# Performance work log

Measured on AMD Instinct MI355X. Metric: run time of the kernel, lower is better.

The kernel has to match this reference:

```python
import jax, jax.numpy as jnp
import numpy as np
import math

D_MODEL, N_HEADS, D_HEAD = 1024, 16, 64
INIT_RANGE = 0.02
IGNORE = -100000.0


def setup_inputs() -> dict:
    key = jax.random.key(0)
    ks = jax.random.split(key, 5)
    x = jax.random.normal(ks[0], (2, 2048, D_MODEL), dtype=jnp.float32)
    W_Q = INIT_RANGE * jax.random.normal(ks[1], (N_HEADS, D_MODEL, D_HEAD), dtype=jnp.float32)
    W_K = INIT_RANGE * jax.random.normal(ks[2], (N_HEADS, D_MODEL, D_HEAD), dtype=jnp.float32)
    W_V = INIT_RANGE * jax.random.normal(ks[3], (N_HEADS, D_MODEL, D_HEAD), dtype=jnp.float32)
    # W_O is contracted as 'n_heads d_head d_model' in the original einsum
    W_O = INIT_RANGE * jax.random.normal(ks[4], (N_HEADS, D_HEAD, D_MODEL), dtype=jnp.float32)
    b_Q = jnp.zeros((N_HEADS, D_HEAD), dtype=jnp.float32)
    b_K = jnp.zeros((N_HEADS, D_HEAD), dtype=jnp.float32)
    b_V = jnp.zeros((N_HEADS, D_HEAD), dtype=jnp.float32)
    b_O = jnp.zeros((D_MODEL,), dtype=jnp.float32)
    return {"normalized_resid_pre": x, "W_Q": W_Q, "b_Q": b_Q, "W_K": W_K, "b_K": b_K,
            "W_V": W_V, "b_V": b_V, "W_O": W_O, "b_O": b_O}


def reference(normalized_resid_pre, W_Q, b_Q, W_K, b_K, W_V, b_V, W_O, b_O):
    x = normalized_resid_pre  # [b, s, d_model]
    q = jnp.einsum('bsd,hde->bshe', x, W_Q) + b_Q  # [b, s, h, d_head]
    k = jnp.einsum('bsd,hde->bshe', x, W_K) + b_K
    v = jnp.einsum('bsd,hde->bshe', x, W_V) + b_V
    scores = jnp.einsum('bqhe,bkhe->bhqk', q, k) / math.sqrt(D_HEAD)
    S = x.shape[1]
    causal = jnp.tril(jnp.ones((S, S), dtype=bool))  # True where allowed
    scores = jnp.where(causal, scores, IGNORE)
    pattern = jax.nn.softmax(scores, axis=-1)  # [b, h, q, k]
    z = jnp.einsum('bhqk,bkhe->bqhe', pattern, v)
    attn_out = jnp.einsum('bqhe,hed->bqd', z, W_O) + b_O
    return attn_out
```

## Files before the change

kernel.cpp:

```cpp
#include <hip/hip_runtime.h>
#include <cstdint>
#include <cstddef>

typedef unsigned short u16;
typedef __bf16 bf16x8 __attribute__((ext_vector_type(8)));
typedef _Float16 f16x4 __attribute__((ext_vector_type(4)));
typedef _Float16 f16x2 __attribute__((ext_vector_type(2)));
typedef float  f32x4  __attribute__((ext_vector_type(4)));
typedef unsigned short u16x8 __attribute__((ext_vector_type(8)));
typedef unsigned short u16x4 __attribute__((ext_vector_type(4)));

#define DM   1024
#define NH   16
#define DH   64
#define SS   2048
#define BSZ  4096
#define NQKV 3072
#define QSCALE 0.18033688011f

__device__ __forceinline__ u16 f2b(float f) {
  unsigned u = __builtin_bit_cast(unsigned, f);
  return (u16)((u + 0x7FFFu + ((u >> 16) & 1u)) >> 16);
}
__device__ __forceinline__ u16 f2h(float f) {
  _Float16 h = (_Float16)f;
  return __builtin_bit_cast(u16, h);
}

__device__ __forceinline__ void gl_lds16(const void* g, void* l) {
  __builtin_amdgcn_global_load_lds(
      (__attribute__((address_space(1))) void*)(void*)g,
      (__attribute__((address_space(3))) void*)l, 16, 0, 0);
}

__global__ __launch_bounds__(256) void prep_all_kernel(
    const float* __restrict__ x, u16* __restrict__ xb,
    const float* __restrict__ Wq, const float* __restrict__ Wk,
    const float* __restrict__ Wv, u16* __restrict__ wqkvt,
    const float* __restrict__ Wo, u16* __restrict__ wot) {
  __shared__ __align__(16) u16 Ts[64 * 72];
  int bid = blockIdx.x, t = threadIdx.x;
  if (bid < 2048) {
    int i = (bid * 256 + t) * 8;
    float4 a = *(const float4*)(x + i);
    float4 b = *(const float4*)(x + i + 4);
    u16x8 o;
    o[0] = f2b(a.x); o[1] = f2b(a.y); o[2] = f2b(a.z); o[3] = f2b(a.w);
    o[4] = f2b(b.x); o[5] = f2b(b.y); o[6] = f2b(b.z); o[7] = f2b(b.w);
    *(u16x8*)(xb + i) = o;
    return;
  }
  if (bid < 2816) {
    int idx = bid - 2048;
    int dt = idx & 15, sl = idx >> 4;
    int proj = sl >> 4, h = sl & 15;
    const float* W = (proj == 0) ? Wq : ((proj == 1) ? Wk : Wv);
    int d0 = dt * 64;
    {
      int ld = t >> 2;
      int ec = (t & 3) * 16;
      const float* src = W + ((size_t)h * DM + d0 + ld) * DH + ec;
      float4 v0 = *(const float4*)(src);
      float4 v1 = *(const float4*)(src + 4);
      float4 v2 = *(const float4*)(src + 8);
      float4 v3 = *(const float4*)(src + 12);
      float vv[16] = {v0.x, v0.y, v0.z, v0.w, v1.x, v1.y, v1.z, v1.w,
                      v2.x, v2.y, v2.z, v2.w, v3.x, v3.y, v3.z, v3.w};
#pragma unroll
      for (int i = 0; i < 16; i++) Ts[(ec + i) * 72 + ld] = f2b(vv[i]);
    }
    __syncthreads();
    {
      int le = t >> 2;
      int dc = (t & 3) * 16;
      int n = proj * DM + h * DH + le;
      u16* dst = wqkvt + (size_t)n * DM + d0 + dc;
      *(u16x8*)(dst)     = *(const u16x8*)&Ts[le * 72 + dc];
      *(u16x8*)(dst + 8) = *(const u16x8*)&Ts[le * 72 + dc + 8];
    }
    return;
  }
  {
    int idx = bid - 2816;
    int dt = idx & 15, h = idx >> 4;
    int d0 = dt * 64;
    {
      int le = t >> 2;
      int dc = (t & 3) * 16;
      const float* src = Wo + ((size_t)h * DH + le) * DM + d0 + dc;
      float4 v0 = *(const float4*)(src);
      float4 v1 = *(const float4*)(src + 4);
      float4 v2 = *(const float4*)(src + 8);
      float4 v3 = *(const float4*)(src + 12);
      float vv[16] = {v0.x, v0.y, v0.z, v0.w, v1.x, v1.y, v1.z, v1.w,
                      v2.x, v2.y, v2.z, v2.w, v3.x, v3.y, v3.z, v3.w};
#pragma unroll
      for (int i = 0; i < 16; i++) Ts[(dc + i) * 72 + le] = f2b(vv[i]);
    }
    __syncthreads();
    {
      int ld = t >> 2;
      int ec = (t & 3) * 16;
      u16* dst = wot + (size_t)(d0 + ld) * DM + h * DH + ec;
      *(u16x8*)(dst)     = *(const u16x8*)&Ts[ld * 72 + ec];
      *(u16x8*)(dst + 8) = *(const u16x8*)&Ts[ld * 72 + ec + 8];
    }
  }
}

__global__ __launch_bounds__(256) void gemm_qkv_kernel(
    const u16* __restrict__ A, const u16* __restrict__ Bt,
    u16* __restrict__ o_q, u16* __restrict__ o_k, u16* __restrict__ o_v,
    const float* __restrict__ c0, const float* __restrict__ c1,
    const float* __restrict__ c2) {
  const int K = DM;
  __shared__ __align__(16) u16 As[128 * 32];
  __shared__ __align__(16) u16 Bs[128 * 32];
  __shared__ __align__(16) u16 Cs[64 * 128];
  int t = threadIdx.x, w = t >> 6, l = t & 63;
  int lr = l & 15, lq = l >> 4;
  int m0 = blockIdx.x * 128, n0 = blockIdx.y * 128;
  int wr = w >> 1, wc = w & 1;
  f32x4 acc[4][4] = {};
  const u16* ga = A + (size_t)(m0 + (t >> 2)) * K + (t & 3) * 8;
  const u16* gb = Bt + (size_t)(n0 + (t >> 2)) * K + (t & 3) * 8;

  for (int k0 = 0; k0 < K; k0 += 32) {
    __syncthreads();
    gl_lds16(ga + k0,           &As[w * 512]);
    gl_lds16(ga + k0 + 64 * K,  &As[2048 + w * 512]);
    gl_lds16(gb + k0,           &Bs[w * 512]);
    gl_lds16(gb + k0 + 64 * K,  &Bs[2048 + w * 512]);
    __syncthreads();
    bf16x8 af[4], bfr[4];
#pragma unroll
    for (int i = 0; i < 4; i++)
      af[i] = *(const bf16x8*)&As[(wr * 64 + i * 16 + lr) * 32 + lq * 8];
#pragma unroll
    for (int j = 0; j < 4; j++)
      bfr[j] = *(const bf16x8*)&Bs[(wc * 64 + j * 16 + lr) * 32 + lq * 8];
#pragma unroll
    for (int i = 0; i < 4; i++)
#pragma unroll
      for (int j = 0; j < 4; j++)
        acc[i][j] = __builtin_amdgcn_mfma_f32_16x16x32_bf16(af[i], bfr[j], acc[i][j], 0, 0, 0);
  }

  int proj = n0 >> 10;
  int r0 = n0 & 1023;
  int h0 = r0 >> 6;
  const float* bp = (proj == 0) ? c0 : ((proj == 1) ? c1 : c2);

#pragma unroll
  for (int p = 0; p < 2; p++) {
    __syncthreads();
    if (wr == p) {
#pragma unroll
      for (int j = 0; j < 4; j++) {
        int nl = wc * 64 + j * 16 + lr;
        float bias = bp[r0 + nl];
#pragma unroll
        for (int i = 0; i < 4; i++) {
#pragma unroll
          for (int g = 0; g < 4; g++) {
            int ml = i * 16 + lq * 4 + g;
            float val = acc[i][j][g] + bias;
            if (proj == 0)      Cs[ml * 128 + nl] = f2b(val * QSCALE);
            else if (proj == 1) Cs[ml * 128 + nl] = f2b(val);
            else                Cs[nl * 64 + ml] = f2h(val);
          }
        }
      }
    }
    __syncthreads();
    int m_base = m0 + p * 64;
    if (proj < 2) {
      int ml = t >> 2, q4 = t & 3;
      int hh = q4 >> 1, e0 = (q4 & 1) * 32;
      int m = m_base + ml, b = m >> 11, s = m & 2047;
      int h = h0 + hh;
      u16* dst = (proj == 0 ? o_q : o_k) + ((size_t)(b * NH + h) * SS + s) * DH + e0;
      const u16* src = &Cs[ml * 128 + hh * 64 + e0];
      *(u16x8*)(dst)      = *(const u16x8*)(src);
      *(u16x8*)(dst + 8)  = *(const u16x8*)(src + 8);
      *(u16x8*)(dst + 16) = *(const u16x8*)(src + 16);
      *(u16x8*)(dst + 24) = *(const u16x8*)(src + 24);
    } else {
      int er = t >> 1, sh = t & 1;
      int hh = er >> 6, e = er & 63;
      int h = h0 + hh;
      int ms = m_base + sh * 32, b = ms >> 11, s = ms & 2047;
      u16* dst = o_v + ((size_t)(b * NH + h) * DH + e) * SS + s;
      const u16* src = &Cs[er * 64 + sh * 32];
      *(u16x8*)(dst)      = *(const u16x8*)(src);
      *(u16x8*)(dst + 8)  = *(const u16x8*)(src + 8);
      *(u16x8*)(dst + 16) = *(const u16x8*)(src + 16);
      *(u16x8*)(dst + 24) = *(const u16x8*)(src + 24);
    }
  }
}

__global__ __launch_bounds__(256) void gemm_o_kernel(
    const u16* __restrict__ A, const u16* __restrict__ Bt,
    const float* __restrict__ bo, float* __restrict__ fout) {
  const int K = DM;
  __shared__ __align__(16) u16 As[128 * 32];
  __shared__ __align__(16) u16 Bs[64 * 32];
  int t = threadIdx.x, w = t >> 6, l = t & 63;
  int lr = l & 15, lq = l >> 4;
  int m0 = blockIdx.x * 128, n0 = blockIdx.y * 64;
  f32x4 acc[2][4] = {};
  const u16* ga = A + (size_t)(m0 + (t >> 2)) * K + (t & 3) * 8;
  const u16* gb = Bt + (size_t)(n0 + (t >> 2)) * K + (t & 3) * 8;

  for (int k0 = 0; k0 < K; k0 += 32) {
    __syncthreads();
    gl_lds16(ga + k0,           &As[w * 512]);
    gl_lds16(ga + k0 + 64 * K,  &As[2048 + w * 512]);
    gl_lds16(gb + k0, &Bs[w * 512]);
    __syncthreads();
    bf16x8 af[2], bfr[4];
#pragma unroll
    for (int i = 0; i < 2; i++)
      af[i] = *(const bf16x8*)&As[(w * 32 + i * 16 + lr) * 32 + lq * 8];
#pragma unroll
    for (int j = 0; j < 4; j++)
      bfr[j] = *(const bf16x8*)&Bs[(j * 16 + lr) * 32 + lq * 8];
#pragma unroll
    for (int i = 0; i < 2; i++)
#pragma unroll
      for (int j = 0; j < 4; j++)
        acc[i][j] = __builtin_amdgcn_mfma_f32_16x16x32_bf16(af[i], bfr[j], acc[i][j], 0, 0, 0);
  }

  int mb = m0 + w * 32 + lq * 4;
  int nb = n0 + lr;
#pragma unroll
  for (int j = 0; j < 4; j++) {
    int n = nb + j * 16;
    float bias = bo[n];
#pragma unroll
    for (int i = 0; i < 2; i++) {
#pragma unroll
      for (int g = 0; g < 4; g++) {
        int m = mb + i * 16 + g;
        fout[(size_t)m * DM + n] = acc[i][j][g] + bias;
      }
    }
  }
}

__global__ __launch_bounds__(512) void attn_kernel(const u16* __restrict__ q_ws,
                                                   const u16* __restrict__ k_ws,
                                                   const u16* __restrict__ vt_ws,
                                                   u16* __restrict__ z_ws) {
  __shared__ __align__(16) u16 KsA[2][64 * 72], VsA[2][64 * 72];
  __shared__ __align__(16) u16 KsB[2][64 * 72], VsB[2][64 * 72];
  __shared__ float lbuf[2][64];

  int t = threadIdx.x;
  int g = t >> 8;
  int tl = t & 255;
  int w4 = tl >> 6;
  int l = t & 63;
  int lr = l & 15, lq = l >> 4;
  int srow = tl >> 3;
  int sc8 = (tl & 7) * 8;

  u16 (*Ks)[64 * 72] = g ? KsB : KsA;
  u16 (*Vs)[64 * 72] = g ? VsB : VsA;

  int bid = blockIdx.x;
  int xcd = bid & 7, idx = bid >> 3;
  int bh = xcd * 4 + (idx & 3);
  int j = idx >> 2;
  const u16* Qb = q_ws + (size_t)bh * SS * DH;
  const u16* Kb = k_ws + (size_t)bh * SS * DH;
  const u16* Vb = vt_ws + (size_t)bh * DH * SS;
  int b = bh >> 4, h16 = bh & 15;

  const f16x4 ones = {(_Float16)1.f, (_Float16)1.f, (_Float16)1.f, (_Float16)1.f};

  for (int half = 0; half < 2; half++) {
    int qt = half ? (31 - j) : j;
    int q0 = qt * 64;
    int nkt = qt + 1;
    int h = nkt >> 1;
    int cnt1 = nkt - h;
    int mycnt = g ? cnt1 : h;
    int base = g ? h : 0;

    int qrow = q0 + w4 * 16 + lr;
    bf16x8 qf0 = *(const bf16x8*)(Qb + (size_t)qrow * DH + lq * 8);
    bf16x8 qf1 = *(const bf16x8*)(Qb + (size_t)qrow * DH + 32 + lq * 8);

    f32x4 accO[4] = {};
    f32x4 accL = {};

    __syncthreads();
    if (mycnt > 0) {
      int k0 = base * 64;
      const u16* kg = Kb + (size_t)(k0 + srow) * DH + sc8;
      const u16* vg = Vb + (size_t)srow * SS + k0 + sc8;
      u16x8 r0 = *(const u16x8*)kg;
      u16x8 r1 = *(const u16x8*)(kg + 32 * DH);
      u16x8 r2 = *(const u16x8*)vg;
      u16x8 r3 = *(const u16x8*)(vg + 32 * SS);
      *(u16x8*)&Ks[0][srow * 72 + sc8] = r0;
      *(u16x8*)&Ks[0][(srow + 32) * 72 + sc8] = r1;
      *(u16x8*)&Vs[0][srow * 72 + sc8] = r2;
      *(u16x8*)&Vs[0][(srow + 32) * 72 + sc8] = r3;
    }

    for (int it = 0; it < cnt1; ++it) {
      __syncthreads();
      bool act = it < mycnt;
      int pb = it & 1;

      u16x8 r0, r1, r2, r3;
      bool have_next = (it + 1 < mycnt);
      if (have_next) {
        int k0n = (base + it + 1) * 64;
        const u16* kg = Kb + (size_t)(k0n + srow) * DH + sc8;
        const u16* vg = Vb + (size_t)srow * SS + k0n + sc8;
        r0 = *(const u16x8*)kg;
        r1 = *(const u16x8*)(kg + 32 * DH);
        r2 = *(const u16x8*)vg;
        r3 = *(const u16x8*)(vg + 32 * SS);
      }

      if (act) {
        f32x4 sc[4];
#pragma unroll
        for (int nt = 0; nt < 4; nt++) {
          bf16x8 kf0 = *(const bf16x8*)&Ks[pb][(nt * 16 + lr) * 72 + lq * 8];
          bf16x8 kf1 = *(const bf16x8*)&Ks[pb][(nt * 16 + lr) * 72 + 32 + lq * 8];
          f32x4 a = {0.f, 0.f, 0.f, 0.f};
          a = __builtin_amdgcn_mfma_f32_16x16x32_bf16(kf0, qf0, a, 0, 0, 0);
          a = __builtin_amdgcn_mfma_f32_16x16x32_bf16(kf1, qf1, a, 0, 0, 0);
          sc[nt] = a;
        }

        if (g == 1 && it == cnt1 - 1) {
          int k0 = (base + it) * 64;
          int gq = q0 + w4 * 16 + lr;
#pragma unroll
          for (int nt = 0; nt < 4; nt++) {
#pragma unroll
            for (int gg = 0; gg < 4; gg++) {
              int gk = k0 + nt * 16 + lq * 4 + gg;
              if (gk > gq) sc[nt][gg] = -1e30f;
            }
          }
        }

        f16x4 pf[4];
#pragma unroll
        for (int nt = 0; nt < 4; nt++) {
          float p0 = exp2f(sc[nt][0]);
          float p1 = exp2f(sc[nt][1]);
          float p2 = exp2f(sc[nt][2]);
          float p3 = exp2f(sc[nt][3]);
          f16x2 e0 = __builtin_bit_cast(f16x2, __builtin_amdgcn_cvt_pkrtz(p0, p1));
          f16x2 e1 = __builtin_bit_cast(f16x2, __builtin_amdgcn_cvt_pkrtz(p2, p3));
          pf[nt][0] = e0[0]; pf[nt][1] = e0[1];
          pf[nt][2] = e1[0]; pf[nt][3] = e1[1];
        }

#pragma unroll
        for (int ks = 0; ks < 4; ks++) {
          accL = __builtin_amdgcn_mfma_f32_16x16x16f16(ones, pf[ks], accL, 0, 0, 0);
#pragma unroll
          for (int et = 0; et < 4; et++) {
            f16x4 vf = *(const f16x4*)&Vs[pb][(et * 16 + lr) * 72 + ks * 16 + lq * 4];
            accO[et] = __builtin_amdgcn_mfma_f32_16x16x16f16(vf, pf[ks], accO[et], 0, 0, 0);
          }
        }
      }

      if (have_next) {
        int nb2 = (it + 1) & 1;
        *(u16x8*)&Ks[nb2][srow * 72 + sc8] = r0;
        *(u16x8*)&Ks[nb2][(srow + 32) * 72 + sc8] = r1;
        *(u16x8*)&Vs[nb2][srow * 72 + sc8] = r2;
        *(u16x8*)&Vs[nb2][(srow + 32) * 72 + sc8] = r3;
      }
    }

    __syncthreads();
    if (lq == 0) lbuf[g][w4 * 16 + lr] = accL[0];
    __syncthreads();
    float inv = 1.0f / (accL[0] + lbuf[1 - g][w4 * 16 + lr]);

    float* cbuf = (float*)VsB[1];
    int gq = q0 + w4 * 16 + lr;
    int crow = w4 * 16 + lr;
    u16* zrow = z_ws + ((size_t)(b * SS + gq)) * DM + h16 * DH;
#pragma unroll
    for (int c = 0; c < 2; c++) {
      if (g == 1) {
#pragma unroll
        for (int e2 = 0; e2 < 2; e2++) {
          int et = 2 * c + e2;
#pragma unroll
          for (int gg = 0; gg < 4; gg++)
            cbuf[crow * 32 + e2 * 16 + lq * 4 + gg] = accO[et][gg];
        }
      }
      __syncthreads();
      if (g == 0) {
#pragma unroll
        for (int e2 = 0; e2 < 2; e2++) {
          int et = 2 * c + e2;
          u16x4 o;
#pragma unroll
          for (int gg = 0; gg < 4; gg++) {
            float v = accO[et][gg] + cbuf[crow * 32 + e2 * 16 + lq * 4 + gg];
            o[gg] = f2b(v * inv);
          }
          *(u16x4*)(zrow + et * 16 + lq * 4) = o;
        }
      }
      __syncthreads();
    }
  }
}

extern "C" void kernel_launch(void* const* d_in, const int* in_sizes, int n_in,
                              void* d_out, int out_size, void* d_ws, size_t ws_size,
                              hipStream_t stream) {
  const float* x  = (const float*)d_in[0];
  const float* Wq = (const float*)d_in[1];
  const float* bq = (const float*)d_in[2];
  const float* Wk = (const float*)d_in[3];
  const float* bk = (const float*)d_in[4];
  const float* Wv = (const float*)d_in[5];
  const float* bv = (const float*)d_in[6];
  const float* Wo = (const float*)d_in[7];
  const float* bo = (const float*)d_in[8];
  float* out = (float*)d_out;

  char* ws = (char*)d_ws;
  const size_t MB = 1u << 20;
  u16* xb    = (u16*)(ws);
  u16* wqkvt = (u16*)(ws + 8 * MB);
  u16* wot   = (u16*)(ws + 14 * MB);
  u16* q_ws  = (u16*)(ws + 16 * MB);
  u16* k_ws  = (u16*)(ws + 24 * MB);
  u16* vt_ws = (u16*)(ws + 32 * MB);
  u16* z_ws  = (u16*)(ws + 40 * MB);

  prep_all_kernel<<<3072, 256, 0, stream>>>(x, xb, Wq, Wk, Wv, wqkvt, Wo, wot);

  gemm_qkv_kernel<<<dim3(BSZ / 128, NQKV / 128), 256, 0, stream>>>(
      xb, wqkvt, q_ws, k_ws, vt_ws, bq, bk, bv);

  attn_kernel<<<512, 512, 0, stream>>>(q_ws, k_ws, vt_ws, z_ws);

  gemm_o_kernel<<<dim3(BSZ / 128, DM / 64), 256, 0, stream>>>(z_ws, wot, bo, out);
}
```

Before: 191.8 us.

## Give each attention block one query tile instead of split-KV paired tiles

```diff
diff --git a/kernel.cpp b/kernel.cpp
--- a/kernel.cpp
+++ b/kernel.cpp
@@ -250,30 +250,23 @@
   }
 }
 
-__global__ __launch_bounds__(512) void attn_kernel(const u16* __restrict__ q_ws,
+__global__ __launch_bounds__(256) void attn_kernel(const u16* __restrict__ q_ws,
                                                    const u16* __restrict__ k_ws,
                                                    const u16* __restrict__ vt_ws,
                                                    u16* __restrict__ z_ws) {
-  __shared__ __align__(16) u16 KsA[2][64 * 72], VsA[2][64 * 72];
-  __shared__ __align__(16) u16 KsB[2][64 * 72], VsB[2][64 * 72];
-  __shared__ float lbuf[2][64];
+  __shared__ __align__(16) u16 Ks[2][64 * 72], Vs[2][64 * 72];
 
   int t = threadIdx.x;
-  int g = t >> 8;
-  int tl = t & 255;
-  int w4 = tl >> 6;
+  int w = t >> 6;
   int l = t & 63;
   int lr = l & 15, lq = l >> 4;
-  int srow = tl >> 3;
-  int sc8 = (tl & 7) * 8;
-
-  u16 (*Ks)[64 * 72] = g ? KsB : KsA;
-  u16 (*Vs)[64 * 72] = g ? VsB : VsA;
+  int srow = t >> 3;
+  int sc8 = (t & 7) * 8;
 
   int bid = blockIdx.x;
   int xcd = bid & 7, idx = bid >> 3;
   int bh = xcd * 4 + (idx & 3);
-  int j = idx >> 2;
+  int qt = 31 - (idx >> 2);
   const u16* Qb = q_ws + (size_t)bh * SS * DH;
   const u16* Kb = k_ws + (size_t)bh * SS * DH;
   const u16* Vb = vt_ws + (size_t)bh * DH * SS;
@@ -281,148 +274,104 @@
 
   const f16x4 ones = {(_Float16)1.f, (_Float16)1.f, (_Float16)1.f, (_Float16)1.f};
 
-  for (int half = 0; half < 2; half++) {
-    int qt = half ? (31 - j) : j;
-    int q0 = qt * 64;
-    int nkt = qt + 1;
-    int h = nkt >> 1;
-    int cnt1 = nkt - h;
-    int mycnt = g ? cnt1 : h;
-    int base = g ? h : 0;
-
-    int qrow = q0 + w4 * 16 + lr;
-    bf16x8 qf0 = *(const bf16x8*)(Qb + (size_t)qrow * DH + lq * 8);
-    bf16x8 qf1 = *(const bf16x8*)(Qb + (size_t)qrow * DH + 32 + lq * 8);
-
-    f32x4 accO[4] = {};
-    f32x4 accL = {};
-
-    __syncthreads();
-    if (mycnt > 0) {
-      int k0 = base * 64;
-      const u16* kg = Kb + (size_t)(k0 + srow) * DH + sc8;
-      const u16* vg = Vb + (size_t)srow * SS + k0 + sc8;
-      u16x8 r0 = *(const u16x8*)kg;
-      u16x8 r1 = *(const u16x8*)(kg + 32 * DH);
-      u16x8 r2 = *(const u16x8*)vg;
-      u16x8 r3 = *(const u16x8*)(vg + 32 * SS);
-      *(u16x8*)&Ks[0][srow * 72 + sc8] = r0;
-      *(u16x8*)&Ks[0][(srow + 32) * 72 + sc8] = r1;
-      *(u16x8*)&Vs[0][srow * 72 + sc8] = r2;
-      *(u16x8*)&Vs[0][(srow + 32) * 72 + sc8] = r3;
-    }
-
-    for (int it = 0; it < cnt1; ++it) {
-      __syncthreads();
-      bool act = it < mycnt;
-      int pb = it & 1;
-
-      u16x8 r0, r1, r2, r3;
-      bool have_next = (it + 1 < mycnt);
-      if (have_next) {
-        int k0n = (base + it + 1) * 64;
-        const u16* kg = Kb + (size_t)(k0n + srow) * DH + sc8;
-        const u16* vg = Vb + (size_t)srow * SS + k0n + sc8;
-        r0 = *(const u16x8*)kg;
-        r1 = *(const u16x8*)(kg + 32 * DH);
-        r2 = *(const u16x8*)vg;
-        r3 = *(const u16x8*)(vg + 32 * SS);
-      }
-
-      if (act) {
-        f32x4 sc[4];
-#pragma unroll
-        for (int nt = 0; nt < 4; nt++) {
-          bf16x8 kf0 = *(const bf16x8*)&Ks[pb][(nt * 16 + lr) * 72 + lq * 8];
-          bf16x8 kf1 = *(const bf16x8*)&Ks[pb][(nt * 16 + lr) * 72 + 32 + lq * 8];
-          f32x4 a = {0.f, 0.f, 0.f, 0.f};
-          a = __builtin_amdgcn_mfma_f32_16x16x32_bf16(kf0, qf0, a, 0, 0, 0);
-          a = __builtin_amdgcn_mfma_f32_16x16x32_bf16(kf1, qf1, a, 0, 0, 0);
-          sc[nt] = a;
-        }
-
-        if (g == 1 && it == cnt1 - 1) {
-          int k0 = (base + it) * 64;
-          int gq = q0 + w4 * 16 + lr;
-#pragma unroll
-          for (int nt = 0; nt < 4; nt++) {
-#pragma unroll
-            for (int gg = 0; gg < 4; gg++) {
-              int gk = k0 + nt * 16 + lq * 4 + gg;
-              if (gk > gq) sc[nt][gg] = -1e30f;
-            }
-          }
-        }
-
-        f16x4 pf[4];
-#pragma unroll
-        for (int nt = 0; nt < 4; nt++) {
-          float p0 = exp2f(sc[nt][0]);
-          float p1 = exp2f(sc[nt][1]);
-          float p2 = exp2f(sc[nt][2]);
-          float p3 = exp2f(sc[nt][3]);
-          f16x2 e0 = __builtin_bit_cast(f16x2, __builtin_amdgcn_cvt_pkrtz(p0, p1));
-          f16x2 e1 = __builtin_bit_cast(f16x2, __builtin_amdgcn_cvt_pkrtz(p2, p3));
-          pf[nt][0] = e0[0]; pf[nt][1] = e0[1];
-          pf[nt][2] = e1[0]; pf[nt][3] = e1[1];
-        }
-
-#pragma unroll
-        for (int ks = 0; ks < 4; ks++) {
-          accL = __builtin_amdgcn_mfma_f32_16x16x16f16(ones, pf[ks], accL, 0, 0, 0);
-#pragma unroll
-          for (int et = 0; et < 4; et++) {
-            f16x4 vf = *(const f16x4*)&Vs[pb][(et * 16 + lr) * 72 + ks * 16 + lq * 4];
-            accO[et] = __builtin_amdgcn_mfma_f32_16x16x16f16(vf, pf[ks], accO[et], 0, 0, 0);
-          }
+  int q0 = qt * 64;
+  int nkt = qt + 1;
+
+  int qrow = q0 + w * 16 + lr;
+  bf16x8 qf0 = *(const bf16x8*)(Qb + (size_t)qrow * DH + lq * 8);
+  bf16x8 qf1 = *(const bf16x8*)(Qb + (size_t)qrow * DH + 32 + lq * 8);
+
+  f32x4 accO[4] = {};
+  f32x4 accL = {};
+
+  {
+    const u16* kg = Kb + (size_t)srow * DH + sc8;
+    const u16* vg = Vb + (size_t)srow * SS + sc8;
+    *(u16x8*)&Ks[0][srow * 72 + sc8] = *(const u16x8*)kg;
+    *(u16x8*)&Ks[0][(srow + 32) * 72 + sc8] = *(const u16x8*)(kg + 32 * DH);
+    *(u16x8*)&Vs[0][srow * 72 + sc8] = *(const u16x8*)vg;
+    *(u16x8*)&Vs[0][(srow + 32) * 72 + sc8] = *(const u16x8*)(vg + 32 * SS);
+  }
+
+  for (int it = 0; it < nkt; ++it) {
+    __syncthreads();
+    int pb = it & 1;
+    bool have_next = (it + 1 < nkt);
+
+    u16x8 r0, r1, r2, r3;
+    if (have_next) {
+      int k0n = (it + 1) * 64;
+      const u16* kg = Kb + (size_t)(k0n + srow) * DH + sc8;
+      const u16* vg = Vb + (size_t)srow * SS + k0n + sc8;
+      r0 = *(const u16x8*)kg;
+      r1 = *(const u16x8*)(kg + 32 * DH);
+      r2 = *(const u16x8*)vg;
+      r3 = *(const u16x8*)(vg + 32 * SS);
+    }
+
+    f32x4 sc[4];
+#pragma unroll
+    for (int nt = 0; nt < 4; nt++) {
+      bf16x8 kf0 = *(const bf16x8*)&Ks[pb][(nt * 16 + lr) * 72 + lq * 8];
+      bf16x8 kf1 = *(const bf16x8*)&Ks[pb][(nt * 16 + lr) * 72 + 32 + lq * 8];
+      f32x4 a = {0.f, 0.f, 0.f, 0.f};
+      a = __builtin_amdgcn_mfma_f32_16x16x32_bf16(kf0, qf0, a, 0, 0, 0);
+      a = __builtin_amdgcn_mfma_f32_16x16x32_bf16(kf1, qf1, a, 0, 0, 0);
+      sc[nt] = a;
+    }
+
+    if (it == nkt - 1) {
+      int k0 = it * 64;
+#pragma unroll
+      for (int nt = 0; nt < 4; nt++) {
+#pragma unroll
+        for (int gg = 0; gg < 4; gg++) {
+          int gk = k0 + nt * 16 + lq * 4 + gg;
+          if (gk > qrow) sc[nt][gg] = -1e30f;
         }
       }
-
-      if (have_next) {
-        int nb2 = (it + 1) & 1;
-        *(u16x8*)&Ks[nb2][srow * 72 + sc8] = r0;
-        *(u16x8*)&Ks[nb2][(srow + 32) * 72 + sc8] = r1;
-        *(u16x8*)&Vs[nb2][srow * 72 + sc8] = r2;
-        *(u16x8*)&Vs[nb2][(srow + 32) * 72 + sc8] = r3;
+    }
+
+    f16x4 pf[4];
+#pragma unroll
+    for (int nt = 0; nt < 4; nt++) {
+      float p0 = exp2f(sc[nt][0]);
+      float p1 = exp2f(sc[nt][1]);
+      float p2 = exp2f(sc[nt][2]);
+      float p3 = exp2f(sc[nt][3]);
+      f16x2 e0 = __builtin_bit_cast(f16x2, __builtin_amdgcn_cvt_pkrtz(p0, p1));
+      f16x2 e1 = __builtin_bit_cast(f16x2, __builtin_amdgcn_cvt_pkrtz(p2, p3));
+      pf[nt][0] = e0[0]; pf[nt][1] = e0[1];
+      pf[nt][2] = e1[0]; pf[nt][3] = e1[1];
+    }
+
+#pragma unroll
+    for (int ks = 0; ks < 4; ks++) {
+      accL = __builtin_amdgcn_mfma_f32_16x16x16f16(ones, pf[ks], accL, 0, 0, 0);
+#pragma unroll
+      for (int et = 0; et < 4; et++) {
+        f16x4 vf = *(const f16x4*)&Vs[pb][(et * 16 + lr) * 72 + ks * 16 + lq * 4];
+        accO[et] = __builtin_amdgcn_mfma_f32_16x16x16f16(vf, pf[ks], accO[et], 0, 0, 0);
       }
     }
 
-    __syncthreads();
-    if (lq == 0) lbuf[g][w4 * 16 + lr] = accL[0];
-    __syncthreads();
-    float inv = 1.0f / (accL[0] + lbuf[1 - g][w4 * 16 + lr]);
-
-    float* cbuf = (float*)VsB[1];
-    int gq = q0 + w4 * 16 + lr;
-    int crow = w4 * 16 + lr;
-    u16* zrow = z_ws + ((size_t)(b * SS + gq)) * DM + h16 * DH;
-#pragma unroll
-    for (int c = 0; c < 2; c++) {
-      if (g == 1) {
-#pragma unroll
-        for (int e2 = 0; e2 < 2; e2++) {
-          int et = 2 * c + e2;
-#pragma unroll
-          for (int gg = 0; gg < 4; gg++)
-            cbuf[crow * 32 + e2 * 16 + lq * 4 + gg] = accO[et][gg];
-        }
-      }
-      __syncthreads();
-      if (g == 0) {
-#pragma unroll
-        for (int e2 = 0; e2 < 2; e2++) {
-          int et = 2 * c + e2;
-          u16x4 o;
-#pragma unroll
-          for (int gg = 0; gg < 4; gg++) {
-            float v = accO[et][gg] + cbuf[crow * 32 + e2 * 16 + lq * 4 + gg];
-            o[gg] = f2b(v * inv);
-          }
-          *(u16x4*)(zrow + et * 16 + lq * 4) = o;
-        }
-      }
-      __syncthreads();
-    }
+    if (have_next) {
+      int nb = (it + 1) & 1;
+      *(u16x8*)&Ks[nb][srow * 72 + sc8] = r0;
+      *(u16x8*)&Ks[nb][(srow + 32) * 72 + sc8] = r1;
+      *(u16x8*)&Vs[nb][srow * 72 + sc8] = r2;
+      *(u16x8*)&Vs[nb][(srow + 32) * 72 + sc8] = r3;
+    }
+  }
+
+  float inv = 1.0f / accL[0];
+  u16* zrow = z_ws + ((size_t)(b * SS + qrow)) * DM + h16 * DH;
+#pragma unroll
+  for (int et = 0; et < 4; et++) {
+    u16x4 o;
+#pragma unroll
+    for (int gg = 0; gg < 4; gg++) o[gg] = f2b(accO[et][gg] * inv);
+    *(u16x4*)(zrow + et * 16 + lq * 4) = o;
   }
 }
 
@@ -455,7 +404,7 @@
   gemm_qkv_kernel<<<dim3(BSZ / 128, NQKV / 128), 256, 0, stream>>>(
       xb, wqkvt, q_ws, k_ws, vt_ws, bq, bk, bv);
 
-  attn_kernel<<<512, 512, 0, stream>>>(q_ws, k_ws, vt_ws, z_ws);
+  attn_kernel<<<1024, 256, 0, stream>>>(q_ws, k_ws, vt_ws, z_ws);
 
   gemm_o_kernel<<<dim3(BSZ / 128, DM / 64), 256, 0, stream>>>(z_ws, wot, bo, out);
 }
```

Result: no change. 189.9 us (-1.0%).
